# Performance work log

Measured on AMD Instinct MI355X. Metric: run time of the kernel, lower is better.

The kernel has to match this reference:

```python
import jax, jax.numpy as jnp
import numpy as np

B, L, D = 2, 2048, 2048
H = 16
DH = D // H  # 128
EPS = 1e-6


def _rope_cos_sin(seq_len, dim, dtype):
    inv_freq = 1.0 / (10000.0 ** (jnp.arange(0, dim, 2, dtype=jnp.float32) / dim))
    t = jnp.arange(seq_len, dtype=jnp.float32)
    freqs = jnp.einsum('i,j->ij', t, inv_freq)          # [L, dim/2]
    emb = jnp.concatenate([freqs, freqs], axis=-1)      # [L, dim]
    return jnp.cos(emb).astype(dtype)[None, None], jnp.sin(emb).astype(dtype)[None, None]


def _rotate_half(x):
    x1, x2 = jnp.split(x, 2, axis=-1)
    return jnp.concatenate([-x2, x1], axis=-1)


def _rms_norm(x, w):
    var = jnp.mean(jnp.square(x), axis=-1, keepdims=True)
    return x * jax.lax.rsqrt(var + EPS) * w


def setup_inputs() -> dict:
    key = jax.random.key(0)
    ks = jax.random.split(key, 4)
    s_in = 1.0 / np.sqrt(D)
    return {
        'x': jax.random.normal(ks[0], (B, L, D), jnp.float32),
        'attention_mask': jnp.zeros((B, 1, 1, L), jnp.bool_),
        'Wqkv': jax.random.normal(ks[1], (D, 3 * D), jnp.float32) * s_in,
        'bqkv': jnp.zeros((3 * D,), jnp.float32),
        'Wout': jax.random.normal(ks[2], (D, D), jnp.float32) * s_in,
        'bout': jnp.zeros((D,), jnp.float32),
        'q_norm_w': jnp.ones((DH,), jnp.float32),
        'k_norm_w': jnp.ones((DH,), jnp.float32),
    }


def reference(x, attention_mask, Wqkv, bqkv, Wout, bout, q_norm_w, k_norm_w):
    b, l, d = x.shape
    qkv = x @ Wqkv + bqkv                                   # [B,L,3D]
    q, k, v = jnp.split(qkv, 3, axis=-1)
    # [B,H,L,DH]
    q = q.reshape(b, l, H, DH).transpose(0, 2, 1, 3)
    k = k.reshape(b, l, H, DH).transpose(0, 2, 1, 3)
    v = v.reshape(b, l, H, DH).transpose(0, 2, 1, 3)

    cos, sin = _rope_cos_sin(l, DH, x.dtype)
    q = q * cos + _rotate_half(q) * sin
    k = k * cos + _rotate_half(k) * sin

    q = _rms_norm(q, q_norm_w)
    k = _rms_norm(k, k_norm_w)

    # SDPA with additive (float-cast) mask, as in the original code
    scale = 1.0 / np.sqrt(DH)
    scores = jnp.einsum('bhqd,bhkd->bhqk', q, k) * scale
    scores = scores + attention_mask.astype(x.dtype)        # broadcast [B,1,1,L]
    attn = jax.nn.softmax(scores, axis=-1)
    out = jnp.einsum('bhqk,bhkd->bhqd', attn, v)            # [B,H,L,DH]

    # zero out masked query rows: padding_mask = mask.transpose(2,3) -> [B,1,L,1]
    padding_mask = jnp.swapaxes(attention_mask, 2, 3)
    out = jnp.where(padding_mask, 0.0, out)

    out = out.transpose(0, 2, 1, 3).reshape(b, l, d)
    return out @ Wout + bout
```

## Files before the change

### kernel.cpp

```cpp
#include <hip/hip_runtime.h>
#include <hip/hip_bf16.h>

typedef __bf16 bf16;
using bf16x8 = __attribute__((ext_vector_type(8))) __bf16;
using bf16x4 = __attribute__((ext_vector_type(4))) __bf16;
using f32x4  = __attribute__((ext_vector_type(4))) float;
using f32x16 = __attribute__((ext_vector_type(16))) float;

#define DEV __device__ __forceinline__

DEV void load_lds16(const void* g, void* l) {
  __builtin_amdgcn_global_load_lds(
      (const __attribute__((address_space(1))) void*)g,
      (__attribute__((address_space(3))) void*)l, 16, 0, 0);
}

__global__ __launch_bounds__(256) void k_prep(
    const float* __restrict__ x, bf16* __restrict__ xb,
    const float* __restrict__ Wq, bf16* __restrict__ wqT,
    const float* __restrict__ Wo, bf16* __restrict__ woT,
    float* __restrict__ invf) {
  __shared__ float t[64][65];
  int bid = blockIdx.x;
  int tid = threadIdx.x;
  if (bid < 4096) {
    long i = ((long)bid * 256 + tid) * 8;
    float4 a = *(const float4*)(x + i);
    float4 b = *(const float4*)(x + i + 4);
    bf16x8 o;
    o[0] = (bf16)a.x; o[1] = (bf16)a.y; o[2] = (bf16)a.z; o[3] = (bf16)a.w;
    o[4] = (bf16)b.x; o[5] = (bf16)b.y; o[6] = (bf16)b.z; o[7] = (bf16)b.w;
    *(bf16x8*)(xb + i) = o;
    return;
  }
  if (bid >= 8192) {
    if (tid < 64) invf[tid] = 1.0f / (float)pow(10000.0, (double)tid / 64.0);
    return;
  }
  const float* in;
  bf16* out;
  int R, C, rb;
  if (bid < 7168) { in = Wq; out = wqT; R = 2048; C = 6144; rb = bid - 4096; }
  else            { in = Wo; out = woT; R = 2048; C = 2048; rb = bid - 7168; }
  int nbc = C >> 6;
  long r0 = (long)(rb / nbc) * 64, c0 = (long)(rb % nbc) * 64;
#pragma unroll
  for (int i = 0; i < 4; ++i) {
    int ch = tid + i * 256;
    int r = ch >> 4, c4 = (ch & 15) * 4;
    float4 v = *(const float4*)(in + (r0 + r) * C + c0 + c4);
    t[r][c4] = v.x; t[r][c4 + 1] = v.y; t[r][c4 + 2] = v.z; t[r][c4 + 3] = v.w;
  }
  __syncthreads();
#pragma unroll
  for (int i = 0; i < 2; ++i) {
    int ch = tid + i * 256;
    int c = ch >> 3, r8 = (ch & 7) * 8;
    bf16x8 o;
#pragma unroll
    for (int j = 0; j < 8; ++j) o[j] = (bf16)t[r8 + j][c];
    *(bf16x8*)(out + (c0 + c) * R + r0 + r8) = o;
  }
}

__global__ __launch_bounds__(512, 1) void k_gemm8q(
    const bf16* __restrict__ A, const bf16* __restrict__ Bt,
    const float* __restrict__ bias,
    const float* __restrict__ invf,
    const float* __restrict__ qw, const float* __restrict__ kw,
    bf16* __restrict__ q_r, bf16* __restrict__ k_r, bf16* __restrict__ v_t) {
  __shared__ __align__(16) bf16 ls[2][2][256 * 64];
  int bid = blockIdx.x;
  { int q = gridDim.x >> 3; bid = (bid & 7) * q + (bid >> 3); }
  const int bm = bid & 15, bn = bid >> 4;
  const int tid = threadIdx.x, lane = tid & 63, w = tid >> 6;
  const int wm = w >> 2, wn = w & 3;
  const int fr = lane & 15, fq = lane >> 4;
  const long abase = (long)bm * 256 * 2048;
  const long bbase = (long)bn * 256 * 2048;
  f32x4 acc[8][4] = {};
  bf16x8 bfv[4][2];

#define STG(op, GP, gb, kt, hf)                                                \
  { _Pragma("unroll") for (int it2 = 0; it2 < 2; ++it2) {                      \
      int g = it2 * 512 + tid;                                                 \
      int rl = g >> 3, u = g & 7;                                              \
      load_lds16(GP + gb + (long)((hf) * 128 + rl) * 2048 + ((kt) << 6)        \
                     + ((u ^ (rl & 7)) << 3),                                  \
                 &ls[op][(kt) & 1][(hf) * 8192 + g * 8]);                      \
  } }

#define PH(qd, slot, STGCODE)                                                  \
  {                                                                            \
    bf16x8 afv[2][2];                                                          \
    _Pragma("unroll") for (int mm = 0; mm < 2; ++mm)                           \
      _Pragma("unroll") for (int kk = 0; kk < 2; ++kk) {                       \
        int R = wm * 128 + ((qd) * 2 + mm) * 16 + fr;                          \
        afv[mm][kk] = *(const bf16x8*)&ls[0][slot]                             \
            [R * 64 + (((kk * 4 + fq) ^ (R & 7)) << 3)];                       \
      }                                                                        \
    if ((qd) == 0) {                                                           \
      _Pragma("unroll") for (int nn = 0; nn < 4; ++nn)                         \
        _Pragma("unroll") for (int kk = 0; kk < 2; ++kk) {                     \
          int R = wn * 64 + nn * 16 + fr;                                      \
          bfv[nn][kk] = *(const bf16x8*)&ls[1][slot]                           \
              [R * 64 + (((kk * 4 + fq) ^ (R & 7)) << 3)];                     \
        }                                                                      \
    }                                                                          \
    STGCODE                                                                    \
    __builtin_amdgcn_s_barrier();                                              \
    asm volatile("s_waitcnt lgkmcnt(0)" ::: "memory");                         \
    __builtin_amdgcn_s_setprio(1);                                             \
    _Pragma("unroll") for (int mm = 0; mm < 2; ++mm)                           \
      _Pragma("unroll") for (int nn = 0; nn < 4; ++nn)                         \
        _Pragma("unroll") for (int kk = 0; kk < 2; ++kk)                       \
          acc[(qd) * 2 + mm][nn] = __builtin_amdgcn_mfma_f32_16x16x32_bf16(    \
              afv[mm][kk], bfv[nn][kk], acc[(qd) * 2 + mm][nn], 0, 0, 0);      \
    __builtin_amdgcn_s_setprio(0);                                             \
    __builtin_amdgcn_s_barrier();                                              \
  }

  STG(1, Bt, bbase, 0, 0) STG(1, Bt, bbase, 0, 1)
  STG(0, A, abase, 0, 0)  STG(0, A, abase, 0, 1)
  STG(1, Bt, bbase, 1, 0) STG(1, Bt, bbase, 1, 1)

  for (int u = 0; u < 16; ++u) {
    const int t = 2 * u;
    asm volatile("s_waitcnt vmcnt(4)" ::: "memory");
    __builtin_amdgcn_s_barrier();
    PH(0, 0, STG(0, A, abase, t + 1, 0))
    PH(1, 0, STG(0, A, abase, t + 1, 1))
    PH(2, 0, if (u < 15) { STG(1, Bt, bbase, t + 2, 0) })
    PH(3, 0, if (u < 15) { STG(1, Bt, bbase, t + 2, 1) })
    if (u < 15) { asm volatile("s_waitcnt vmcnt(4)" ::: "memory"); }
    else        { asm volatile("s_waitcnt vmcnt(0)" ::: "memory"); }
    __builtin_amdgcn_s_barrier();
    PH(0, 1, if (u < 15) { STG(0, A, abase, t + 2, 0) })
    PH(1, 1, if (u < 15) { STG(0, A, abase, t + 2, 1) })
    PH(2, 1, if (u < 15) { STG(1, Bt, bbase, t + 3, 0) })
    PH(3, 1, if (u < 15) { STG(1, Bt, bbase, t + 3, 1) })
  }
#undef PH
#undef STG

  bf16* tile = &ls[0][0][0];
  const int b = bm >> 3, l0 = (bm & 7) << 8;

  if (bn < 16) {
#pragma unroll
    for (int n = 0; n < 4; ++n) {
      int col = wn * 64 + n * 16 + fr;
      float bv = bias[bn * 256 + col];
#pragma unroll
      for (int m = 0; m < 8; ++m)
#pragma unroll
        for (int r = 0; r < 4; ++r) {
          int row = wm * 128 + m * 16 + fq * 4 + r;
          tile[row * 256 + (col ^ ((row & 7) << 3))] = (bf16)(acc[m][n][r] + bv);
        }
    }
    __syncthreads();
    const float* wv = (bn < 8) ? qw : kw;
    bf16* dst0 = (bn < 8) ? q_r : k_r;
    const int tc = tid & 15, hh = (tid >> 4) & 1, rgrp = tid >> 5, i8 = tc * 8;
    const int hg = (bn & 7) * 2 + hh;
    const bool lo = i8 < 64;
    float wvv[8], invv[8];
#pragma unroll
    for (int j = 0; j < 8; ++j) wvv[j] = wv[i8 + j];
#pragma unroll
    for (int j = 0; j < 8; ++j) invv[j] = invf[(i8 + j) & 63];
#pragma unroll
    for (int it = 0; it < 16; ++it) {
      int row = it * 16 + rgrp;
      float fl = (float)(l0 + row);
      float cc[8], sn[8];
#pragma unroll
      for (int j = 0; j < 8; ++j) __sincosf(fl * invv[j], &sn[j], &cc[j]);
      int colb = hh * 128 + i8;
      bf16x8 xv = *(const bf16x8*)&tile[row * 256 + (colb ^ ((row & 7) << 3))];
      float v[8], p[8], rr[8];
      float ss = 0.f;
#pragma unroll
      for (int j = 0; j < 8; ++j) v[j] = (float)xv[j];
#pragma unroll
      for (int j = 0; j < 8; ++j) p[j] = __shfl_xor(v[j], 8);
#pragma unroll
      for (int j = 0; j < 8; ++j) {
        rr[j] = lo ? v[j] * cc[j] - p[j] * sn[j] : v[j] * cc[j] + p[j] * sn[j];
        ss += rr[j] * rr[j];
      }
      ss += __shfl_xor(ss, 1);
      ss += __shfl_xor(ss, 2);
      ss += __shfl_xor(ss, 4);
      ss += __shfl_xor(ss, 8);
      float inv = rsqrtf(ss * (1.f / 128.f) + 1e-6f);
      bf16x8 ov;
#pragma unroll
      for (int j = 0; j < 8; ++j) ov[j] = (bf16)(rr[j] * inv * wvv[j]);
      *(bf16x8*)(dst0 + ((long)((b * 16 + hg) * 2048 + (l0 + row))) * 128 + i8) = ov;
    }
  } else {
#pragma unroll
    for (int n = 0; n < 4; ++n) {
      int col = wn * 64 + n * 16 + fr;
      float bv = bias[bn * 256 + col];
#pragma unroll
      for (int m = 0; m < 8; ++m)
#pragma unroll
        for (int r = 0; r < 4; ++r) {
          int row = wm * 128 + m * 16 + fq * 4 + r;
          tile[col * 256 + (row ^ ((col & 7) << 3))] = (bf16)(acc[m][n][r] + bv);
        }
    }
    __syncthreads();
#pragma unroll
    for (int it = 0; it < 16; ++it) {
      int ch = it * 512 + tid;
      int d = ch >> 5, l8 = (ch & 31) * 8;
      int hg = (bn - 16) * 2 + (d >> 7), dl = d & 127;
      bf16x8 vv = *(const bf16x8*)&tile[d * 256 + (l8 ^ ((d & 7) << 3))];
      *(bf16x8*)(v_t + ((long)((b * 16 + hg) * 128 + dl)) * 2048 + l0 + l8) = vv;
    }
  }
}

__global__ __launch_bounds__(256) void k_gemm_bt(
    const bf16* __restrict__ A, const bf16* __restrict__ Bt,
    const float* __restrict__ bias, float* __restrict__ C,
    int M, int N, int K) {
  __shared__ __align__(16) bf16 lA[128 * 64];
  __shared__ __align__(16) bf16 lB[128 * 64];
  int bid = blockIdx.x;
  if ((gridDim.x & 7) == 0) {
    int q = gridDim.x >> 3;
    bid = (bid & 7) * q + (bid >> 3);
  }
  int nbn = N >> 7;
  int bm = bid / nbn, bn = bid % nbn;
  const int tid = threadIdx.x, lane = tid & 63, wid = tid >> 6;
  const int wr = wid >> 1, wc = wid & 1;
  const int fr = lane & 15, fq = lane >> 4;
  const long abase = (long)bm * 128 * K, bbase = (long)bn * 128 * K;
  f32x4 acc[4][4] = {};

  for (int k0 = 0; k0 < K; k0 += 64) {
    __syncthreads();
#pragma unroll
    for (int it = 0; it < 4; ++it) {
      int ch = it * 256 + tid;
      int r = ch >> 3, u = ch & 7;
      load_lds16(A + abase + (long)r * K + k0 + ((u ^ (r & 7)) << 3), &lA[ch * 8]);
    }
#pragma unroll
    for (int it = 0; it < 4; ++it) {
      int ch = it * 256 + tid;
      int r = ch >> 3, u = ch & 7;
      load_lds16(Bt + bbase + (long)r * K + k0 + ((u ^ (r & 7)) << 3), &lB[ch * 8]);
    }
    __syncthreads();
    bf16x8 af[4][2], bf_[4][2];
#pragma unroll
    for (int m = 0; m < 4; ++m) {
      int R = wr * 64 + m * 16 + fr;
#pragma unroll
      for (int kk = 0; kk < 2; ++kk)
        af[m][kk] = *(const bf16x8*)&lA[R * 64 + (((kk * 4 + fq) ^ (R & 7)) << 3)];
    }
#pragma unroll
    for (int n = 0; n < 4; ++n) {
      int R = wc * 64 + n * 16 + fr;
#pragma unroll
      for (int kk = 0; kk < 2; ++kk)
        bf_[n][kk] = *(const bf16x8*)&lB[R * 64 + (((kk * 4 + fq) ^ (R & 7)) << 3)];
    }
#pragma unroll
    for (int m = 0; m < 4; ++m)
#pragma unroll
      for (int n = 0; n < 4; ++n)
#pragma unroll
        for (int kk = 0; kk < 2; ++kk)
          acc[m][n] = __builtin_amdgcn_mfma_f32_16x16x32_bf16(af[m][kk], bf_[n][kk],
                                                              acc[m][n], 0, 0, 0);
  }
#pragma unroll
  for (int n = 0; n < 4; ++n) {
    int col = bn * 128 + wc * 64 + n * 16 + fr;
    float bv = bias[col];
#pragma unroll
    for (int m = 0; m < 4; ++m) {
      int row0 = bm * 128 + wr * 64 + m * 16 + fq * 4;
#pragma unroll
      for (int r = 0; r < 4; ++r)
        C[(long)(row0 + r) * N + col] = acc[m][n][r] + bv;
    }
  }
}

__global__ __launch_bounds__(512, 1) void k_attn(
    const bf16* __restrict__ q_r, const bf16* __restrict__ k_r,
    const bf16* __restrict__ v_t, const unsigned char* __restrict__ amask,
    bf16* __restrict__ attno) {
  __shared__ __align__(16) bf16 lK[2][64 * 128];
  __shared__ __align__(16) bf16 lV[3][128 * 64];
  __shared__ int sAny;
  const int tid = threadIdx.x, lane = tid & 63, w = tid >> 6;
  const int hi = lane >> 5, q31 = lane & 31;
  const int bh = blockIdx.x & 31, qt = blockIdx.x >> 5;
  const int b = bh >> 4, h = bh & 15;
  const long hbase = (long)bh * 2048 * 128;
  const int q0 = qt * 256 + w * 32;
  const unsigned char* mb = amask + b * 2048;

  if (tid == 0) sAny = 0;
  __syncthreads();
  {
    unsigned mv = *(const unsigned*)(mb + tid * 4);
    if (mv) sAny = 1;
  }

  bf16x8 qf[8];
#pragma unroll
  for (int ksl = 0; ksl < 8; ++ksl)
    qf[ksl] = *(const bf16x8*)(q_r + hbase + (long)(q0 + q31) * 128 + ksl * 16 + hi * 8);

  f32x16 o[4] = {};
  float m_run = -1e30f, l_run = 0.f;
  const float SC2 = 0.08838834764831845f * 1.4426950408889634f;
  const float L2E = 1.4426950408889634f;

#define STAGE_K(buf, kv0)                                                            \
  {                                                                                  \
    _Pragma("unroll") for (int it = 0; it < 2; ++it) {                               \
      int g = it * 512 + w * 64 + lane;                                              \
      int r = g >> 4, u = g & 15;                                                    \
      load_lds16(k_r + hbase + (long)((kv0) + r) * 128 + ((u ^ (r & 7)) << 3),       \
                 &lK[buf][(it * 512 + w * 64) * 8]);                                 \
    }                                                                                \
  }
#define STAGE_V(buf, kv0)                                                            \
  {                                                                                  \
    _Pragma("unroll") for (int it = 0; it < 2; ++it) {                               \
      int g = it * 512 + w * 64 + lane;                                              \
      int r = g >> 3, u = g & 7;                                                     \
      load_lds16(v_t + hbase + (long)r * 2048 + (kv0) + ((u ^ (r & 7)) << 3),        \
                 &lV[buf][(it * 512 + w * 64) * 8]);                                 \
    }                                                                                \
  }

  STAGE_K(0, 0) STAGE_V(0, 0) STAGE_K(1, 64) STAGE_V(1, 64)
  __syncthreads();
  const bool maskAny = sAny != 0;

  f32x16 st0 = {}, st1 = {};
#pragma unroll
  for (int ksl = 0; ksl < 8; ++ksl) {
    const int u = ksl * 2 + hi;
    bf16x8 kf0 = *(const bf16x8*)&lK[0][q31 * 128 + ((u ^ (q31 & 7)) << 3)];
    bf16x8 kf1 = *(const bf16x8*)&lK[0][(32 + q31) * 128 + ((u ^ (q31 & 7)) << 3)];
    st0 = __builtin_amdgcn_mfma_f32_32x32x16_bf16(kf0, qf[ksl], st0, 0, 0, 0);
    st1 = __builtin_amdgcn_mfma_f32_32x32x16_bf16(kf1, qf[ksl], st1, 0, 0, 0);
  }
  __syncthreads();

  for (int t = 0; t < 32; ++t) {
    const int kv0 = t << 6;
    if (t + 2 < 32) {
      STAGE_K(t & 1, kv0 + 128)
      STAGE_V((t + 2) % 3, kv0 + 128)
    }

    f32x16 sn0 = {}, sn1 = {};
    if (t < 31) {
      const bf16* kb = lK[(t + 1) & 1];
#pragma unroll
      for (int ksl = 0; ksl < 8; ++ksl) {
        const int u = ksl * 2 + hi;
        bf16x8 kf0 = *(const bf16x8*)&kb[q31 * 128 + ((u ^ (q31 & 7)) << 3)];
        bf16x8 kf1 = *(const bf16x8*)&kb[(32 + q31) * 128 + ((u ^ (q31 & 7)) << 3)];
        sn0 = __builtin_amdgcn_mfma_f32_32x32x16_bf16(kf0, qf[ksl], sn0, 0, 0, 0);
        sn1 = __builtin_amdgcn_mfma_f32_32x32x16_bf16(kf1, qf[ksl], sn1, 0, 0, 0);
      }
    }

#pragma unroll
    for (int i = 0; i < 16; ++i) { st0[i] *= SC2; st1[i] *= SC2; }
    if (maskAny) {
#pragma unroll
      for (int i = 0; i < 16; ++i) {
        int c = (i & 3) + 8 * (i >> 2) + 4 * hi;
        if (mb[kv0 + c]) st0[i] += L2E;
        if (mb[kv0 + 32 + c]) st1[i] += L2E;
      }
    }
    float tm = st0[0];
#pragma unroll
    for (int i = 1; i < 16; ++i) tm = fmaxf(tm, st0[i]);
#pragma unroll
    for (int i = 0; i < 16; ++i) tm = fmaxf(tm, st1[i]);
    tm = fmaxf(tm, __shfl_xor(tm, 32));

    if (!__all(tm <= m_run + 8.f)) {
      float mn = fmaxf(m_run, tm);
      float corr = exp2f(m_run - mn);
      m_run = mn;
      l_run *= corr;
#pragma unroll
      for (int i = 0; i < 16; ++i) {
        float cr = __shfl(corr, (i & 3) + 8 * (i >> 2) + 4 * hi);
#pragma unroll
        for (int dt = 0; dt < 4; ++dt) o[dt][i] *= cr;
      }
    }

    float rs = 0.f;
#pragma unroll
    for (int i = 0; i < 16; ++i) { st0[i] = exp2f(st0[i] - m_run); rs += st0[i]; }
#pragma unroll
    for (int i = 0; i < 16; ++i) { st1[i] = exp2f(st1[i] - m_run); rs += st1[i]; }
    rs += __shfl_xor(rs, 32);
    l_run += rs;

    union UU { bf16x4 v; uint2 u; };
    union U8 { bf16x8 v; uint4 u; };
    bf16x8 pa[4];
#define MKPA(pidx, STX, bb)                                                          \
  {                                                                                  \
    UU plo, phi;                                                                     \
    plo.v = (bf16x4){(bf16)STX[bb], (bf16)STX[(bb) + 1], (bf16)STX[(bb) + 2],        \
                     (bf16)STX[(bb) + 3]};                                           \
    phi.v = (bf16x4){(bf16)STX[(bb) + 4], (bf16)STX[(bb) + 5], (bf16)STX[(bb) + 6],  \
                     (bf16)STX[(bb) + 7]};                                           \
    unsigned sx = hi ? plo.u.x : phi.u.x, sy = hi ? plo.u.y : phi.u.y;               \
    unsigned rx = (unsigned)__shfl_xor((int)sx, 32), ry = (unsigned)__shfl_xor((int)sy, 32); \
    U8 f;                                                                            \
    f.u.x = hi ? rx : plo.u.x; f.u.y = hi ? ry : plo.u.y;                            \
    f.u.z = hi ? phi.u.x : rx; f.u.w = hi ? phi.u.y : ry;                            \
    pa[pidx] = f.v;                                                                  \
  }
    MKPA(0, st0, 0) MKPA(1, st0, 8) MKPA(2, st1, 0) MKPA(3, st1, 8)
#undef MKPA

    const bf16* vb3 = lV[t % 3];
#pragma unroll
    for (int dt = 0; dt < 4; ++dt) {
      const int dr = dt * 32 + q31;
#pragma unroll
      for (int ks = 0; ks < 4; ++ks) {
        const int u = ks * 2 + hi;
        bf16x8 vb = *(const bf16x8*)&vb3[dr * 64 + ((u ^ (dr & 7)) << 3)];
        o[dt] = __builtin_amdgcn_mfma_f32_32x32x16_bf16(pa[ks], vb, o[dt], 0, 0, 0);
      }
    }

    __syncthreads();
    st0 = sn0;
    st1 = sn1;
  }
#undef STAGE_K
#undef STAGE_V

  float invl = 1.f / l_run;
#pragma unroll
  for (int i = 0; i < 16; ++i) {
    int q = (i & 3) + 8 * (i >> 2) + 4 * hi;
    int qrow = q0 + q;
    float inv = __shfl(invl, q);
    float zm = inv;
    if (maskAny) { if (mb[qrow]) zm = 0.f; }
#pragma unroll
    for (int dt = 0; dt < 4; ++dt)
      attno[(long)(b * 2048 + qrow) * 2048 + h * 128 + dt * 32 + q31] = (bf16)(o[dt][i] * zm);
  }
}

extern "C" void kernel_launch(void* const* d_in, const int* in_sizes, int n_in,
                              void* d_out, int out_size, void* d_ws, size_t ws_size,
                              hipStream_t stream) {
  const float* x = (const float*)d_in[0];
  const unsigned char* amask = (const unsigned char*)d_in[1];
  const float* Wqkv = (const float*)d_in[2];
  const float* bqkv = (const float*)d_in[3];
  const float* Wout = (const float*)d_in[4];
  const float* bout = (const float*)d_in[5];
  const float* qw = (const float*)d_in[6];
  const float* kw = (const float*)d_in[7];
  float* out = (float*)d_out;
  char* ws = (char*)d_ws;

  bf16* xb   = (bf16*)(ws);
  bf16* wqT  = (bf16*)(ws + 16777216);
  bf16* woT  = (bf16*)(ws + 41943040);
  bf16* q_r  = (bf16*)(ws + 100663296);
  bf16* k_r  = (bf16*)(ws + 117440512);
  bf16* v_t  = (bf16*)(ws + 134217728);
  float* invf = (float*)(ws + 150994944);
  bf16* attno = xb;

  k_prep<<<8193, 256, 0, stream>>>(x, xb, Wqkv, wqT, Wout, woT, invf);
  k_gemm8q<<<384, 512, 0, stream>>>(xb, wqT, bqkv, invf, qw, kw, q_r, k_r, v_t);
  k_attn<<<256, 512, 0, stream>>>(q_r, k_r, v_t, amask, attno);
  k_gemm_bt<<<32 * 16, 256, 0, stream>>>(attno, woT, bout, out, 4096, 2048, 2048);
}
```

Baseline: 289.3 us.

## Replace output projection GEMM with triple-buffered 8-wave 128x256 tile kernel

The output projection GEMM moves from a single-buffered 256-thread 128x128 tile kernel to a 512-thread kernel with 128x256 tiles and a three-stage LDS ring. Global-to-LDS loads for tile t+2 are issued while MFMAs run on tile t, with explicit vmcnt waits, split barriers and setprio around the MFMA phases. The aim is to hide load latency and raise reuse per block. In exchange the grid drops to 256 blocks at one block per CU, and correctness now depends on hand-counted wait counts.

```diff
diff --git a/kernel.cpp b/kernel.cpp
--- a/kernel.cpp
+++ b/kernel.cpp
@@ -225,74 +225,116 @@
   }
 }
 
-__global__ __launch_bounds__(256) void k_gemm_bt(
+__global__ __launch_bounds__(512, 1) void k_g8out(
     const bf16* __restrict__ A, const bf16* __restrict__ Bt,
     const float* __restrict__ bias, float* __restrict__ C,
     int M, int N, int K) {
-  __shared__ __align__(16) bf16 lA[128 * 64];
-  __shared__ __align__(16) bf16 lB[128 * 64];
+  __shared__ __align__(16) bf16 ls[3 * 8192 + 3 * 16384];
+  bf16* lsA = ls;
+  bf16* lsB = ls + 3 * 8192;
   int bid = blockIdx.x;
-  if ((gridDim.x & 7) == 0) {
-    int q = gridDim.x >> 3;
-    bid = (bid & 7) * q + (bid >> 3);
-  }
-  int nbn = N >> 7;
-  int bm = bid / nbn, bn = bid % nbn;
-  const int tid = threadIdx.x, lane = tid & 63, wid = tid >> 6;
-  const int wr = wid >> 1, wc = wid & 1;
+  { int q = gridDim.x >> 3; bid = (bid & 7) * q + (bid >> 3); }
+  const int nbm = M >> 7;
+  const int bm = bid % nbm, bn = bid / nbm;
+  const int tid = threadIdx.x, lane = tid & 63, w = tid >> 6;
+  const int wm = w >> 2, wn = w & 3;
   const int fr = lane & 15, fq = lane >> 4;
-  const long abase = (long)bm * 128 * K, bbase = (long)bn * 128 * K;
+  const long abase = (long)bm * 128 * K;
+  const long bbase = (long)bn * 256 * K;
+  const int NT = K >> 6;
   f32x4 acc[4][4] = {};
-
-  for (int k0 = 0; k0 < K; k0 += 64) {
-    __syncthreads();
-#pragma unroll
-    for (int it = 0; it < 4; ++it) {
-      int ch = it * 256 + tid;
-      int r = ch >> 3, u = ch & 7;
-      load_lds16(A + abase + (long)r * K + k0 + ((u ^ (r & 7)) << 3), &lA[ch * 8]);
-    }
-#pragma unroll
-    for (int it = 0; it < 4; ++it) {
-      int ch = it * 256 + tid;
-      int r = ch >> 3, u = ch & 7;
-      load_lds16(Bt + bbase + (long)r * K + k0 + ((u ^ (r & 7)) << 3), &lB[ch * 8]);
-    }
-    __syncthreads();
-    bf16x8 af[4][2], bf_[4][2];
+  bf16x8 bfv[4][2];
+
+#define STGA(sl, kt)                                                           \
+  { _Pragma("unroll") for (int i2 = 0; i2 < 2; ++i2) {                         \
+      int g = i2 * 512 + tid;                                                  \
+      int rl = g >> 3, uu = g & 7;                                             \
+      load_lds16(A + abase + (long)rl * K + ((kt) << 6) + ((uu ^ (rl & 7)) << 3), \
+                 &lsA[(sl) * 8192 + g * 8]); } }
+#define STGB(sl, kt, i0, i1)                                                   \
+  { _Pragma("unroll") for (int i2 = i0; i2 < i1; ++i2) {                       \
+      int g = i2 * 512 + tid;                                                  \
+      int rl = g >> 3, uu = g & 7;                                             \
+      load_lds16(Bt + bbase + (long)rl * K + ((kt) << 6) + ((uu ^ (rl & 7)) << 3), \
+                 &lsB[(sl) * 16384 + g * 8]); } }
+
+  STGA(0, 0) STGB(0, 0, 0, 4)
+  STGA(1, 1) STGB(1, 1, 0, 4)
+
+  for (int t = 0; t < NT; ++t) {
+    const int sl = t % 3, s2 = (t + 2) % 3;
+    if (t < NT - 1) asm volatile("s_waitcnt vmcnt(6)" ::: "memory");
+    else            asm volatile("s_waitcnt vmcnt(0)" ::: "memory");
+    __builtin_amdgcn_s_barrier();
+    {
+      bf16x8 af0[2][2];
+#pragma unroll
+      for (int mm = 0; mm < 2; ++mm)
+#pragma unroll
+        for (int kk = 0; kk < 2; ++kk) {
+          int R = wm * 64 + mm * 16 + fr;
+          af0[mm][kk] = *(const bf16x8*)&lsA[sl * 8192 + R * 64 + (((kk * 4 + fq) ^ (R & 7)) << 3)];
+        }
+#pragma unroll
+      for (int nn = 0; nn < 4; ++nn)
+#pragma unroll
+        for (int kk = 0; kk < 2; ++kk) {
+          int R = wn * 64 + nn * 16 + fr;
+          bfv[nn][kk] = *(const bf16x8*)&lsB[sl * 16384 + R * 64 + (((kk * 4 + fq) ^ (R & 7)) << 3)];
+        }
+      if (t + 2 < NT) { STGA(s2, t + 2) STGB(s2, t + 2, 0, 2) }
+      __builtin_amdgcn_s_barrier();
+      asm volatile("s_waitcnt lgkmcnt(0)" ::: "memory");
+      __builtin_amdgcn_s_setprio(1);
+#pragma unroll
+      for (int mm = 0; mm < 2; ++mm)
+#pragma unroll
+        for (int nn = 0; nn < 4; ++nn)
+#pragma unroll
+          for (int kk = 0; kk < 2; ++kk)
+            acc[mm][nn] = __builtin_amdgcn_mfma_f32_16x16x32_bf16(af0[mm][kk], bfv[nn][kk],
+                                                                  acc[mm][nn], 0, 0, 0);
+      __builtin_amdgcn_s_setprio(0);
+      __builtin_amdgcn_s_barrier();
+    }
+    {
+      bf16x8 af1[2][2];
+#pragma unroll
+      for (int mm = 0; mm < 2; ++mm)
+#pragma unroll
+        for (int kk = 0; kk < 2; ++kk) {
+          int R = wm * 64 + (2 + mm) * 16 + fr;
+          af1[mm][kk] = *(const bf16x8*)&lsA[sl * 8192 + R * 64 + (((kk * 4 + fq) ^ (R & 7)) << 3)];
+        }
+      if (t + 2 < NT) { STGB(s2, t + 2, 2, 4) }
+      __builtin_amdgcn_s_barrier();
+      asm volatile("s_waitcnt lgkmcnt(0)" ::: "memory");
+      __builtin_amdgcn_s_setprio(1);
+#pragma unroll
+      for (int mm = 0; mm < 2; ++mm)
+#pragma unroll
+        for (int nn = 0; nn < 4; ++nn)
+#pragma unroll
+          for (int kk = 0; kk < 2; ++kk)
+            acc[2 + mm][nn] = __builtin_amdgcn_mfma_f32_16x16x32_bf16(af1[mm][kk], bfv[nn][kk],
+                                                                      acc[2 + mm][nn], 0, 0, 0);
+      __builtin_amdgcn_s_setprio(0);
+      __builtin_amdgcn_s_barrier();
+    }
+  }
+#undef STGA
+#undef STGB
+
+#pragma unroll
+  for (int nn = 0; nn < 4; ++nn) {
+    int col = bn * 256 + wn * 64 + nn * 16 + fr;
+    float bv = bias[col];
 #pragma unroll
     for (int m = 0; m < 4; ++m) {
-      int R = wr * 64 + m * 16 + fr;
-#pragma unroll
-      for (int kk = 0; kk < 2; ++kk)
-        af[m][kk] = *(const bf16x8*)&lA[R * 64 + (((kk * 4 + fq) ^ (R & 7)) << 3)];
-    }
-#pragma unroll
-    for (int n = 0; n < 4; ++n) {
-      int R = wc * 64 + n * 16 + fr;
-#pragma unroll
-      for (int kk = 0; kk < 2; ++kk)
-        bf_[n][kk] = *(const bf16x8*)&lB[R * 64 + (((kk * 4 + fq) ^ (R & 7)) << 3)];
-    }
-#pragma unroll
-    for (int m = 0; m < 4; ++m)
-#pragma unroll
-      for (int n = 0; n < 4; ++n)
-#pragma unroll
-        for (int kk = 0; kk < 2; ++kk)
-          acc[m][n] = __builtin_amdgcn_mfma_f32_16x16x32_bf16(af[m][kk], bf_[n][kk],
-                                                              acc[m][n], 0, 0, 0);
-  }
-#pragma unroll
-  for (int n = 0; n < 4; ++n) {
-    int col = bn * 128 + wc * 64 + n * 16 + fr;
-    float bv = bias[col];
-#pragma unroll
-    for (int m = 0; m < 4; ++m) {
-      int row0 = bm * 128 + wr * 64 + m * 16 + fq * 4;
+      int row0 = bm * 128 + wm * 64 + m * 16 + fq * 4;
 #pragma unroll
       for (int r = 0; r < 4; ++r)
-        C[(long)(row0 + r) * N + col] = acc[m][n][r] + bv;
+        C[(long)(row0 + r) * N + col] = acc[m][nn][r] + bv;
     }
   }
 }
@@ -500,5 +542,5 @@
   k_prep<<<8193, 256, 0, stream>>>(x, xb, Wqkv, wqT, Wout, woT, invf);
   k_gemm8q<<<384, 512, 0, stream>>>(xb, wqT, bqkv, invf, qw, kw, q_r, k_r, v_t);
   k_attn<<<256, 512, 0, stream>>>(q_r, k_r, v_t, amask, attno);
-  k_gemm_bt<<<32 * 16, 256, 0, stream>>>(attno, woT, bout, out, 4096, 2048, 2048);
+  k_g8out<<<256, 512, 0, stream>>>(attno, woT, bout, out, 4096, 2048, 2048);
 }
```

Result: no change. 289.4 us, median of 2 (+0.0%).
